# Optimization experiments

Hardware: AMD Instinct MI355X
Metric: run time of the kernel (lower is better)

## Reference

```python
import jax, jax.numpy as jnp
import numpy as np

V, D, N, M, H, W, K = 97, 512, 128, 64, 8, 8, 3
HALF = K // 2
DH = D // H
RPL = M + 3 + K   # key(M) + beta + gate + shift(K) + gamma = 70
WPL = RPL + 2 * M # + erase(M) + add(M) = 198
B, T = 32, 128


def _ln(x, g, b):
    mu = x.mean(-1, keepdims=True)
    var = ((x - mu) ** 2).mean(-1, keepdims=True)
    return (x - mu) / jnp.sqrt(var + 1e-5) * g + b


def _addressing(key, beta, gate, shift, gamma, prev_w, memory):
    # key [B,M], beta/gate/gamma [B,1], shift [B,K], prev_w [B,N], memory [B,N,M]
    eps = 1e-12
    kn = key / (jnp.linalg.norm(key, axis=-1, keepdims=True) + eps)
    mn = memory / (jnp.linalg.norm(memory, axis=-1, keepdims=True) + eps)
    cos = jnp.einsum('bnm,bm->bn', mn, kn)
    wc = jax.nn.softmax(jax.nn.softplus(beta) * cos, axis=-1)
    g = jax.nn.sigmoid(gate)
    wg = g * wc + (1.0 - g) * prev_w
    s = jax.nn.softmax(shift, axis=-1)
    shifted = sum(s[:, k:k + 1] * jnp.roll(wg, k - HALF, axis=-1) for k in range(K))
    gp = 1.0 + jax.nn.softplus(gamma)
    wt = (shifted + eps) ** gp
    return wt / (wt.sum(-1, keepdims=True) + eps)


def setup_inputs() -> dict:
    key = jax.random.key(0)
    ks = jax.random.split(key, 16)
    s = 0.05
    return {
        'x': jax.random.randint(ks[0], (B, T), 0, V),
        'emb': jax.random.normal(ks[1], (V, D)) * 0.02,
        'W_in': jax.random.normal(ks[2], (D, D + M)) * s,
        'b_in': jnp.zeros((D,)),
        'W_qkv': jax.random.normal(ks[3], (3 * D, D)) * s,
        'b_qkv': jnp.zeros((3 * D,)),
        'W_o': jax.random.normal(ks[4], (D, D)) * s,
        'b_o': jnp.zeros((D,)),
        'ln1_g': jnp.ones((D,)), 'ln1_b': jnp.zeros((D,)),
        'W_ff1': jax.random.normal(ks[5], (4 * D, D)) * s,
        'b_ff1': jnp.zeros((4 * D,)),
        'W_ff2': jax.random.normal(ks[6], (D, 4 * D)) * s,
        'b_ff2': jnp.zeros((D,)),
        'ln2_g': jnp.ones((D,)), 'ln2_b': jnp.zeros((D,)),
        'W_tok': jax.random.normal(ks[7], (V, D)) * s,
        'b_tok': jnp.zeros((V,)),
        'W_read': jax.random.normal(ks[8], (RPL, D)) * s,
        'b_read': jnp.zeros((RPL,)),
        'W_write': jax.random.normal(ks[9], (WPL, D)) * s,
        'b_write': jnp.zeros((WPL,)),
    }


def _forward(x, emb, W_in, b_in, W_qkv, b_qkv, W_o, b_o, ln1_g, ln1_b,
             W_ff1, b_ff1, W_ff2, b_ff2, ln2_g, ln2_b, W_tok, b_tok,
             W_read, b_read, W_write, b_write):
    Wq, Wk, Wv = W_qkv[:D], W_qkv[D:2 * D], W_qkv[2 * D:]
    bq, bk, bv = b_qkv[:D], b_qkv[D:2 * D], b_qkv[2 * D:]
    scale = 1.0 / np.sqrt(DH)

    def step(carry, x_t):
        memory, rw, ww, cache, t = carry
        tok = emb[x_t]                                   # [B,D]
        r = jnp.einsum('bn,bnm->bm', rw, memory)         # read vector [B,M]
        wide = jnp.concatenate([tok, r], -1)             # [B,D+M]
        xp = wide @ W_in.T + b_in                        # [B,D]
        q = xp[None]                                     # [1,B,D]
        # kv buffer: cache (detached) + current q, truncated to last W
        kbuf = jnp.concatenate([cache, q], 0)[-W:]       # [W,B,D]
        valid = jnp.arange(W) >= W - jnp.minimum(t + 1, W)
        qh = (xp @ Wq.T + bq).reshape(-1, H, DH)         # [B,H,DH]
        kh = (kbuf @ Wk.T + bk).reshape(W, -1, H, DH)    # [W,B,H,DH]
        vh = (kbuf @ Wv.T + bv).reshape(W, -1, H, DH)
        scores = jnp.einsum('bhe,wbhe->bhw', qh, kh) * scale
        scores = jnp.where(valid[None, None, :], scores, -jnp.inf)
        attn = jax.nn.softmax(scores, axis=-1)
        ctx = jnp.einsum('bhw,wbhe->bhe', attn, vh).reshape(-1, D)
        attn_out = ctx @ W_o.T + b_o
        x2 = _ln(xp + attn_out, ln1_g, ln1_b)
        ff = jax.nn.gelu(x2 @ W_ff1.T + b_ff1, approximate=False) @ W_ff2.T + b_ff2
        out = _ln(x2 + ff, ln2_g, ln2_b)
        logits = out @ W_tok.T + b_tok
        # read head addressing (RH=1)
        rp = out @ W_read.T + b_read
        new_rw = _addressing(rp[:, :M], rp[:, M:M + 1], rp[:, M + 1:M + 2],
                             rp[:, M + 2:M + 2 + K], rp[:, M + 2 + K:M + 3 + K],
                             rw, memory)
        # write head addressing + erase/add (WH=1)
        wp = out @ W_write.T + b_write
        new_ww = _addressing(wp[:, :M], wp[:, M:M + 1], wp[:, M + 1:M + 2],
                             wp[:, M + 2:M + 2 + K], wp[:, M + 2 + K:M + 3 + K],
                             ww, memory)
        erase = jax.nn.sigmoid(wp[:, RPL:RPL + M])       # [B,M]
        add = jnp.tanh(wp[:, RPL + M:])                  # [B,M]
        new_mem = memory * (1.0 - new_ww[:, :, None] * erase[:, None, :]) \
                  + new_ww[:, :, None] * add[:, None, :]
        new_cache = jax.lax.stop_gradient(jnp.concatenate([cache, q], 0)[-W:])
        return (new_mem, new_rw, new_ww, new_cache, t + 1), logits

    Bv = x.shape[0]
    mem0 = jnp.zeros((Bv, N, M), jnp.float32)
    w0 = jnp.zeros((Bv, N), jnp.float32).at[:, 0].set(1.0)
    cache0 = jnp.zeros((W, Bv, D), jnp.float32)
    carry0 = (mem0, w0, w0, cache0, jnp.int32(0))
    _, logits = jax.lax.scan(step, carry0, x.T)          # [T,B,V]
    return jnp.transpose(logits, (1, 0, 2))              # [B,T,V]


def reference(x, emb, W_in, b_in, W_qkv, b_qkv, W_o, b_o, ln1_g, ln1_b,
              W_ff1, b_ff1, W_ff2, b_ff2, ln2_g, ln2_b, W_tok, b_tok,
              W_read, b_read, W_write, b_write):
    return _forward(x, emb, W_in, b_in, W_qkv, b_qkv, W_o, b_o, ln1_g, ln1_b,
                    W_ff1, b_ff1, W_ff2, b_ff2, ln2_g, ln2_b, W_tok, b_tok,
                    W_read, b_read, W_write, b_write)
```

## Files before the change

### kernel.cpp

```cpp
#include <hip/hip_runtime.h>
#include <math.h>

static constexpr int Tc = 128, Vc = 97;

static constexpr size_t T_FQ  = 0;
static constexpr size_t BF    = T_FQ + (size_t)576*1536;
static constexpr size_t T_IN  = BF + 1536;
static constexpr size_t T_O   = T_IN + (size_t)576*512;
static constexpr size_t T_FF1 = T_O + (size_t)512*512;
static constexpr size_t T_FF2 = T_FF1 + (size_t)512*2048;
static constexpr size_t T_TOK = T_FF2 + (size_t)2048*512;
static constexpr size_t T_RW  = T_TOK + (size_t)512*128;
static constexpr size_t ARENA = T_RW + (size_t)512*288;
static constexpr size_t TEAM_STRIDE = 8704;
static constexpr size_t A_YP = 0;
static constexpr size_t A_OP = 4096;
static constexpr size_t A_RWP = 8192;
static constexpr size_t FLG = ARENA + (size_t)32*TEAM_STRIDE;

__device__ __forceinline__ float softplusf_(float x) { return x > 20.f ? x : log1pf(expf(x)); }
__device__ __forceinline__ float sigmoidf_(float x) { return 1.f / (1.f + expf(-x)); }

__device__ __forceinline__ float wsum(float v) {
#pragma unroll
  for (int o = 1; o < 64; o <<= 1) v += __shfl_xor(v, o);
  return v;
}
__device__ __forceinline__ float wmax(float v) {
#pragma unroll
  for (int o = 1; o < 64; o <<= 1) v = fmaxf(v, __shfl_xor(v, o));
  return v;
}

__device__ __forceinline__ void st_llc(float* p, float v) {
  __hip_atomic_store(p, v, __ATOMIC_RELAXED, __HIP_MEMORY_SCOPE_SYSTEM);
}
__device__ __forceinline__ float ld_llc(const float* p) {
  return __hip_atomic_load(p, __ATOMIC_RELAXED, __HIP_MEMORY_SCOPE_SYSTEM);
}
__device__ __forceinline__ void st_flag(int* p, int v) {
  __hip_atomic_store(p, v, __ATOMIC_RELAXED, __HIP_MEMORY_SCOPE_SYSTEM);
}
__device__ __forceinline__ int ld_flag(const int* p) {
  return __hip_atomic_load(p, __ATOMIC_RELAXED, __HIP_MEMORY_SCOPE_SYSTEM);
}

#define PUBF(stage)                                                      \
  do {                                                                   \
    asm volatile("s_waitcnt vmcnt(0)" ::: "memory");                     \
    __syncthreads();                                                     \
    if (tid == 0) st_flag(flg + (stage)*128 + sq*16, t + 1);             \
  } while (0)

#define WAITF(stage, need)                                               \
  do {                                                                   \
    if (tid < 8) {                                                       \
      while (ld_flag(flg + (stage)*128 + tid*16) < (need))               \
        __builtin_amdgcn_s_sleep(1);                                     \
    }                                                                    \
    __syncthreads();                                                     \
    asm volatile("" ::: "memory");                                       \
  } while (0)

template <int NCH, int CH, int NG, int SF4>
__device__ __forceinline__ void mvp(const float* __restrict__ wbase,
                                    const float* __restrict__ src,
                                    float* part, int tid) {
  const int cs = tid / NG, g = tid % NG;
  const float4* __restrict__ w4 =
      reinterpret_cast<const float4*>(wbase + (size_t)cs * CH * (SF4 * 4)) + g;
  const float* __restrict__ v = src + cs * CH;
  float a0 = 0.f, a1 = 0.f, a2 = 0.f, a3 = 0.f;
#pragma unroll 8
  for (int c = 0; c < CH; ++c) {
    float4 w = w4[(size_t)c * SF4];
    float vv = v[c];
    a0 += vv * w.x; a1 += vv * w.y; a2 += vv * w.z; a3 += vv * w.w;
  }
  *reinterpret_cast<float4*>(part + tid * 4) = make_float4(a0, a1, a2, a3);
}

__global__ __launch_bounds__(256) void k_init(const float* __restrict__ W_in,
                                              const float* __restrict__ W_qkv,
                                              const float* __restrict__ W_o,
                                              const float* __restrict__ W_ff1,
                                              const float* __restrict__ W_ff2,
                                              const float* __restrict__ W_tok,
                                              const float* __restrict__ W_read,
                                              const float* __restrict__ W_write,
                                              const float* __restrict__ b_qkv,
                                              const float* __restrict__ b_in,
                                              float* __restrict__ ws) {
  const size_t tid = (size_t)blockIdx.x * 256 + threadIdx.x;
  const size_t nth = (size_t)gridDim.x * 256;
  for (size_t i = tid; i < (size_t)576*512; i += nth) {
    size_t c = i >> 9, j = i & 511;
    ws[T_IN + i] = W_in[j * 576 + c];
  }
  for (size_t i = tid; i < (size_t)512*512; i += nth) {
    size_t e = i >> 9, j = i & 511;
    ws[T_O + i] = W_o[j * 512 + e];
  }
  for (size_t i = tid; i < (size_t)512*2048; i += nth) {
    size_t d = i >> 11, f = i & 2047;
    ws[T_FF1 + i] = W_ff1[f * 512 + d];
  }
  for (size_t i = tid; i < (size_t)2048*512; i += nth) {
    size_t k = i >> 9, j = i & 511;
    ws[T_FF2 + i] = W_ff2[j * 2048 + k];
  }
  for (size_t i = tid; i < (size_t)512*128; i += nth) {
    size_t d = i >> 7, j = i & 127;
    int qq = (int)(j >> 4), i2 = (int)(j & 15);
    int v = qq * 13 + i2;
    ws[T_TOK + i] = (i2 < 13 && v < 97) ? W_tok[(size_t)v * 512 + d] : 0.f;
  }
  for (size_t i = tid; i < (size_t)512*288; i += nth) {
    size_t d = i / 288, j = i % 288;
    int qq = (int)(j / 36), i2 = (int)(j % 36);
    int idx = qq * 34 + i2;
    float val = 0.f;
    if (i2 < 34 && idx < 268)
      val = (idx < 70) ? W_read[(size_t)idx * 512 + d] : W_write[(size_t)(idx - 70) * 512 + d];
    ws[T_RW + i] = val;
  }
  for (size_t j = tid; j < 1536; j += nth) {
    float a = b_qkv[j];
    const float* r = W_qkv + j * 512;
    for (int d = 0; d < 512; ++d) a += r[d] * b_in[d];
    ws[BF + j] = a;
  }
  for (size_t i = tid; i < (size_t)32 * TEAM_STRIDE; i += nth) ws[ARENA + i] = 0.f;
  for (size_t i = tid; i < 32768; i += nth) ((int*)(ws + FLG))[i] = 0;
}

__global__ __launch_bounds__(256) void k_fuse(const float* __restrict__ W_qkv,
                                              const float* __restrict__ W_in,
                                              float* __restrict__ ws) {
  __shared__ float As[32][64];
  __shared__ float Bs[32][96];
  const int cb = blockIdx.x % 9, jb = blockIdx.x / 9;
  const int c0 = cb * 64, j0 = jb * 96;
  const int tid = threadIdx.x;
  float acc[24];
#pragma unroll
  for (int u = 0; u < 24; ++u) acc[u] = 0.f;
  for (int d0 = 0; d0 < 512; d0 += 32) {
    __syncthreads();
    for (int i = tid; i < 32 * 64; i += 256) { int dd = i >> 6, cc = i & 63; As[dd][cc] = W_in[(size_t)(d0 + dd) * 576 + c0 + cc]; }
    for (int i = tid; i < 32 * 96; i += 256) { int jj = i >> 5, dd = i & 31; Bs[dd][jj] = W_qkv[(size_t)(j0 + jj) * 512 + d0 + dd]; }
    __syncthreads();
    const int tc = tid & 63, jbase = (tid >> 6) * 24;
    for (int dd = 0; dd < 32; ++dd) {
      float a = As[dd][tc];
#pragma unroll
      for (int u = 0; u < 24; ++u) acc[u] += a * Bs[dd][jbase + u];
    }
  }
  const int tc = tid & 63, jbase = (tid >> 6) * 24;
#pragma unroll
  for (int u = 0; u < 24; ++u)
    ws[T_FQ + (size_t)(c0 + tc) * 1536 + j0 + jbase + u] = acc[u];
}

__global__ __launch_bounds__(512) void k_main(
    const int* __restrict__ x, const float* __restrict__ emb,
    const float* __restrict__ b_in, const float* __restrict__ b_o,
    const float* __restrict__ ln1g, const float* __restrict__ ln1b,
    const float* __restrict__ b_ff1, const float* __restrict__ b_ff2,
    const float* __restrict__ ln2g, const float* __restrict__ ln2b,
    const float* __restrict__ b_tok,
    const float* __restrict__ b_read, const float* __restrict__ b_write,
    float* __restrict__ ws, float* __restrict__ dout) {
  const float* __restrict__ wt = ws;
  const int wg = blockIdx.x, tid = threadIdx.x;
  const int sq = wg & 7, b = wg >> 3;
  const int wv = tid >> 6, ln = tid & 63;
  float* ar = ws + ARENA + (size_t)b * TEAM_STRIDE;
  int* flg = (int*)(ws + FLG) + b * 1024;

  __shared__ float memS[128 * 64];
  __shared__ float kcS[8 * 64], vcS[8 * 64];
  __shared__ float rwvS[128], wwvS[128], wwnS[128];
  __shared__ float rvec[64];
  __shared__ float wideS[576];
  __shared__ float xpSl[64];
  __shared__ float qhS[64];
  __shared__ float scoresS[8], awS[8];
  __shared__ float ctxH[64];
  __shared__ float yS[512], x2S[512], oS[512], onS[512];
  __shared__ float hSl[256];
  __shared__ __align__(16) float part[2048];
  __shared__ float rwpS[272];
  __shared__ float cosS[256];
  __shared__ float redA[8], redB[8];
  __shared__ float eS[64], aS[64];

  for (int i = tid; i < 8192; i += 512) memS[i] = 0.f;
  if (tid < 128) { float v0 = (tid == 0) ? 1.f : 0.f; rwvS[tid] = v0; wwvS[tid] = v0; }
  __syncthreads();

  for (int t = 0; t < Tc; ++t) {
    {
      float a = 0.f;
#pragma unroll
      for (int k2 = 0; k2 < 16; ++k2) { int n = wv * 16 + k2; a += rwvS[n] * memS[n * 64 + ln]; }
      part[wv * 64 + ln] = a;
    }
    __syncthreads();
    if (tid < 64) {
      float s = 0.f;
#pragma unroll
      for (int p = 0; p < 8; ++p) s += part[p * 64 + tid];
      rvec[tid] = s;
    }
    __syncthreads();
    const int tok = x[b * Tc + t];
    for (int i = tid; i < 576; i += 512)
      wideS[i] = (i < 512) ? emb[(size_t)tok * 512 + i] : rvec[i - 512];
    __syncthreads();

    const int slot = t & 7;
    for (int p3 = 0; p3 < 3; ++p3) {
      mvp<32, 18, 16, 384>(wt + T_FQ + p3 * 512 + 64 * sq, wideS, part, tid);
      __syncthreads();
      if (tid < 64) {
        float s = wt[BF + p3 * 512 + 64 * sq + tid];
#pragma unroll
        for (int cs = 0; cs < 32; ++cs) s += part[cs * 64 + tid];
        if (p3 == 0) qhS[tid] = s;
        else if (p3 == 1) kcS[slot * 64 + tid] = s;
        else vcS[slot * 64 + tid] = s;
      }
      __syncthreads();
    }
    mvp<32, 18, 16, 128>(wt + T_IN + 64 * sq, wideS, part, tid);
    __syncthreads();
    if (tid < 64) {
      float s = b_in[64 * sq + tid];
#pragma unroll
      for (int cs = 0; cs < 32; ++cs) s += part[cs * 64 + tid];
      xpSl[tid] = s;
    }
    __syncthreads();

    {
      int st = t - 7 + wv;
      float c = 0.f;
      if (st >= 0) c = qhS[ln] * kcS[(st & 7) * 64 + ln];
      c = wsum(c);
      if (ln == 0) scoresS[wv] = (st >= 0) ? c * 0.125f : -INFINITY;
    }
    __syncthreads();
    if (tid == 0) {
      float mx = -INFINITY;
      for (int j = 0; j < 8; ++j) mx = fmaxf(mx, scoresS[j]);
      float e[8], ssum = 0.f;
      for (int j = 0; j < 8; ++j) { e[j] = expf(scoresS[j] - mx); ssum += e[j]; }
      float inv = 1.f / ssum;
      for (int j = 0; j < 8; ++j) awS[j] = e[j] * inv;
    }
    __syncthreads();
    if (tid < 64) {
      float a = 0.f;
#pragma unroll
      for (int j = 0; j < 8; ++j) {
        int st = t - 7 + j;
        if (st >= 0) a += awS[j] * vcS[(st & 7) * 64 + tid];
      }
      ctxH[tid] = a;
    }
    __syncthreads();

    mvp<4, 16, 128, 128>(wt + T_O + (size_t)64 * sq * 512, ctxH, part, tid);
    __syncthreads();
    {
      float s = 0.f;
#pragma unroll
      for (int cs = 0; cs < 4; ++cs) s += part[cs * 512 + tid];
      if ((tid >> 6) == sq) s += xpSl[tid & 63];
      st_llc(ar + A_YP + sq * 512 + tid, s);
    }
    PUBF(0);
    WAITF(0, t + 1);
    {
      float s = b_o[tid];
#pragma unroll
      for (int q2 = 0; q2 < 8; ++q2) s += ld_llc(ar + A_YP + q2 * 512 + tid);
      yS[tid] = s;
    }
    __syncthreads();
    {
      float v = yS[tid];
      float a = wsum(v), b2 = wsum(v * v);
      if (ln == 0) { redA[wv] = a; redB[wv] = b2; }
      __syncthreads();
      float sa = 0.f, sb = 0.f;
#pragma unroll
      for (int i2 = 0; i2 < 8; ++i2) { sa += redA[i2]; sb += redB[i2]; }
      float mu = sa * (1.f / 512.f);
      float var = sb * (1.f / 512.f) - mu * mu;
      float rstd = rsqrtf(var + 1e-5f);
      x2S[tid] = (yS[tid] - mu) * rstd * ln1g[tid] + ln1b[tid];
    }
    __syncthreads();

    mvp<8, 64, 64, 512>(wt + T_FF1 + 256 * sq, x2S, part, tid);
    __syncthreads();
    if (tid < 256) {
      float s = b_ff1[256 * sq + tid];
#pragma unroll
      for (int cs = 0; cs < 8; ++cs) s += part[cs * 256 + tid];
      hSl[tid] = 0.5f * s * (1.f + erff(s * 0.70710678118654752f));
    }
    __syncthreads();

    mvp<4, 64, 128, 128>(wt + T_FF2 + (size_t)256 * sq * 512, hSl, part, tid);
    __syncthreads();
    {
      float s = 0.f;
#pragma unroll
      for (int cs = 0; cs < 4; ++cs) s += part[cs * 512 + tid];
      st_llc(ar + A_OP + sq * 512 + tid, s);
    }
    PUBF(1);
    WAITF(1, t + 1);
    {
      float s = b_ff2[tid] + x2S[tid];
#pragma unroll
      for (int q2 = 0; q2 < 8; ++q2) s += ld_llc(ar + A_OP + q2 * 512 + tid);
      oS[tid] = s;
    }
    __syncthreads();
    {
      float v = oS[tid];
      float a = wsum(v), b2 = wsum(v * v);
      if (ln == 0) { redA[wv] = a; redB[wv] = b2; }
      __syncthreads();
      float sa = 0.f, sb = 0.f;
#pragma unroll
      for (int i2 = 0; i2 < 8; ++i2) { sa += redA[i2]; sb += redB[i2]; }
      float mu = sa * (1.f / 512.f);
      float var = sb * (1.f / 512.f) - mu * mu;
      float rstd = rsqrtf(var + 1e-5f);
      onS[tid] = (oS[tid] - mu) * rstd * ln2g[tid] + ln2b[tid];
    }
    __syncthreads();

    if (tid < 288) {
      const int cs = tid / 9, g = tid % 9;
      const float4* __restrict__ w4 =
          reinterpret_cast<const float4*>(wt + T_RW + (size_t)(cs * 16) * 288 + 36 * sq) + g;
      const float* __restrict__ v = onS + cs * 16;
      float a0 = 0.f, a1 = 0.f, a2 = 0.f, a3 = 0.f;
#pragma unroll
      for (int c = 0; c < 16; ++c) {
        float4 w = w4[(size_t)c * 72];
        float vv = v[c];
        a0 += vv * w.x; a1 += vv * w.y; a2 += vv * w.z; a3 += vv * w.w;
      }
      *reinterpret_cast<float4*>(part + cs * 36 + g * 4) = make_float4(a0, a1, a2, a3);
    }
    __syncthreads();
    if (tid < 34) {
      int idx = 34 * sq + tid;
      if (idx < 268) {
        float s = (idx < 70) ? b_read[idx] : b_write[idx - 70];
#pragma unroll
        for (int cs = 0; cs < 32; ++cs) s += part[cs * 36 + tid];
        st_llc(ar + A_RWP + idx, s);
      }
    }
    PUBF(2);
    if (tid < 128) {
      const int cs = tid >> 2, g = tid & 3;
      const float4* __restrict__ w4 =
          reinterpret_cast<const float4*>(wt + T_TOK + (size_t)(cs * 16) * 128 + 16 * sq) + g;
      const float* __restrict__ v = onS + cs * 16;
      float a0 = 0.f, a1 = 0.f, a2 = 0.f, a3 = 0.f;
#pragma unroll
      for (int c = 0; c < 16; ++c) {
        float4 w = w4[(size_t)c * 32];
        float vv = v[c];
        a0 += vv * w.x; a1 += vv * w.y; a2 += vv * w.z; a3 += vv * w.w;
      }
      *reinterpret_cast<float4*>(part + tid * 4) = make_float4(a0, a1, a2, a3);
    }
    __syncthreads();
    if (tid < 13) {
      int v = 13 * sq + tid;
      if (v < Vc) {
        float s = b_tok[v];
#pragma unroll
        for (int cs = 0; cs < 32; ++cs) s += part[cs * 16 + tid];
        dout[((size_t)b * Tc + t) * Vc + v] = s;
      }
    }
    WAITF(2, t + 1);
    if (tid < 268) rwpS[tid] = ld_llc(ar + A_RWP + tid);
    __syncthreads();

    for (int p = 0; p < 32; ++p) {
      int idx = wv * 32 + p;
      int ksel = idx >> 7, row = idx & 127;
      const float* key = ksel ? (rwpS + 70) : rwpS;
      float m = memS[row * 64 + ln];
      float pp = m * key[ln], qq = m * m;
#pragma unroll
      for (int o = 1; o < 64; o <<= 1) { pp += __shfl_xor(pp, o); qq += __shfl_xor(qq, o); }
      if (ln == 0) cosS[idx] = pp / (sqrtf(qq) + 1e-12f);
    }
    __syncthreads();
    if (wv < 2) {
      const float* P = wv ? (rwpS + 70) : rwpS;
      const float* cosb = cosS + wv * 128;
      float* prevw = wv ? wwvS : rwvS;
      float kk = P[ln];
      float kn2 = wsum(kk * kk);
      float kinv = 1.f / (sqrtf(kn2) + 1e-12f);
      float beta = softplusf_(P[64]);
      float g = sigmoidf_(P[65]);
      float sh0 = P[66], sh1 = P[67], sh2 = P[68];
      float m3 = fmaxf(sh0, fmaxf(sh1, sh2));
      float es0 = expf(sh0 - m3), es1 = expf(sh1 - m3), es2 = expf(sh2 - m3);
      float i3 = 1.f / (es0 + es1 + es2);
      es0 *= i3; es1 *= i3; es2 *= i3;
      float gp = 1.f + softplusf_(P[69]);
      float v0 = beta * cosb[ln] * kinv, v1 = beta * cosb[64 + ln] * kinv;
      float mx = wmax(fmaxf(v0, v1));
      float e0 = expf(v0 - mx), e1 = expf(v1 - mx);
      float einv = 1.f / wsum(e0 + e1);
      float w0 = g * e0 * einv + (1.f - g) * prevw[ln];
      float w1 = g * e1 * einv + (1.f - g) * prevw[64 + ln];
      float w0m = __shfl(w0, (ln + 63) & 63), w1m = __shfl(w1, (ln + 63) & 63);
      float w0p = __shfl(w0, (ln + 1) & 63),  w1p = __shfl(w1, (ln + 1) & 63);
      float prev0 = (ln == 0)  ? w1m : w0m;
      float next0 = (ln == 63) ? w1p : w0p;
      float prev1 = (ln == 0)  ? w0m : w1m;
      float next1 = (ln == 63) ? w0p : w1p;
      float t0 = es0 * next0 + es1 * w0 + es2 * prev0;
      float t1 = es0 * next1 + es1 * w1 + es2 * prev1;
      float wt0 = powf(t0 + 1e-12f, gp), wt1 = powf(t1 + 1e-12f, gp);
      float winv = 1.f / (wsum(wt0 + wt1) + 1e-12f);
      w0 = wt0 * winv; w1 = wt1 * winv;
      prevw[ln] = w0; prevw[64 + ln] = w1;
      if (wv) { wwnS[ln] = w0; wwnS[64 + ln] = w1; }
    } else if (wv == 2) {
      eS[ln] = sigmoidf_(rwpS[140 + ln]);
      aS[ln] = tanhf(rwpS[204 + ln]);
    }
    __syncthreads();
    for (int i = tid; i < 8192; i += 512) {
      int n = i >> 6, m = i & 63;
      float wn = wwnS[n];
      memS[i] = memS[i] * (1.f - wn * eS[m]) + wn * aS[m];
    }
    __syncthreads();
  }
}

extern "C" void kernel_launch(void* const* d_in, const int* in_sizes, int n_in,
                              void* d_out, int out_size, void* d_ws, size_t ws_size,
                              hipStream_t stream) {
  (void)in_sizes; (void)n_in; (void)out_size; (void)ws_size;
  const int* x = (const int*)d_in[0];
  const float* emb = (const float*)d_in[1];
  const float* W_in = (const float*)d_in[2];
  const float* b_in = (const float*)d_in[3];
  const float* W_qkv = (const float*)d_in[4];
  const float* b_qkv = (const float*)d_in[5];
  const float* W_o = (const float*)d_in[6];
  const float* b_o = (const float*)d_in[7];
  const float* ln1g = (const float*)d_in[8];
  const float* ln1b = (const float*)d_in[9];
  const float* W_ff1 = (const float*)d_in[10];
  const float* b_ff1 = (const float*)d_in[11];
  const float* W_ff2 = (const float*)d_in[12];
  const float* b_ff2 = (const float*)d_in[13];
  const float* ln2g = (const float*)d_in[14];
  const float* ln2b = (const float*)d_in[15];
  const float* W_tok = (const float*)d_in[16];
  const float* b_tok = (const float*)d_in[17];
  const float* W_read = (const float*)d_in[18];
  const float* b_read = (const float*)d_in[19];
  const float* W_write = (const float*)d_in[20];
  const float* b_write = (const float*)d_in[21];
  float* ws = (float*)d_ws;
  float* out = (float*)d_out;

  hipLaunchKernelGGL(k_init, dim3(512), dim3(256), 0, stream,
                     W_in, W_qkv, W_o, W_ff1, W_ff2, W_tok, W_read, W_write,
                     b_qkv, b_in, ws);
  hipLaunchKernelGGL(k_fuse, dim3(144), dim3(256), 0, stream, W_qkv, W_in, ws);
  hipLaunchKernelGGL(k_main, dim3(256), dim3(512), 0, stream,
                     x, emb, b_in, b_o, ln1g, ln1b, b_ff1, b_ff2,
                     ln2g, ln2b, b_tok, b_read, b_write, ws, out);
}
```

Baseline: 6.163 ms.

## Fuse QKV and input projections into one pass and batch weight loads

Merges the three Q/K/V matrix-vector passes and the W_in projection into a single loop, so each thread reads all four weight streams against the same input element. This cuts four rounds of sync-and-reduce down to one, and the partial-sum buffer grows to hold four outputs. The other matvecs now use a helper that issues eight float4 loads before doing the FMAs, which gives more memory-level parallelism. The launch bounds also ask for two blocks per CU, which can constrain registers and add spills. The larger shared-memory buffer may limit occupancy.

```diff
diff --git a/kernel.cpp b/kernel.cpp
--- a/kernel.cpp
+++ b/kernel.cpp
@@ -62,22 +62,28 @@
     asm volatile("" ::: "memory");                                       \
   } while (0)
 
-template <int NCH, int CH, int NG, int SF4>
-__device__ __forceinline__ void mvp(const float* __restrict__ wbase,
-                                    const float* __restrict__ src,
-                                    float* part, int tid) {
-  const int cs = tid / NG, g = tid % NG;
-  const float4* __restrict__ w4 =
-      reinterpret_cast<const float4*>(wbase + (size_t)cs * CH * (SF4 * 4)) + g;
-  const float* __restrict__ v = src + cs * CH;
+template <int CH, int SF4>
+__device__ __forceinline__ float4 dotw4(const float4* __restrict__ w4,
+                                        const float* __restrict__ v) {
   float a0 = 0.f, a1 = 0.f, a2 = 0.f, a3 = 0.f;
-#pragma unroll 8
-  for (int c = 0; c < CH; ++c) {
-    float4 w = w4[(size_t)c * SF4];
-    float vv = v[c];
+#pragma unroll
+  for (int c0 = 0; c0 + 8 <= CH; c0 += 8) {
+    float4 w[8];
+#pragma unroll
+    for (int j = 0; j < 8; ++j) w[j] = w4[(size_t)(c0 + j) * SF4];
+#pragma unroll
+    for (int j = 0; j < 8; ++j) {
+      float vv = v[c0 + j];
+      a0 += vv * w[j].x; a1 += vv * w[j].y; a2 += vv * w[j].z; a3 += vv * w[j].w;
+    }
+  }
+#pragma unroll
+  for (int cr = CH & ~7; cr < CH; ++cr) {
+    float4 w = w4[(size_t)cr * SF4];
+    float vv = v[cr];
     a0 += vv * w.x; a1 += vv * w.y; a2 += vv * w.z; a3 += vv * w.w;
   }
-  *reinterpret_cast<float4*>(part + tid * 4) = make_float4(a0, a1, a2, a3);
+  return make_float4(a0, a1, a2, a3);
 }
 
 __global__ __launch_bounds__(256) void k_init(const float* __restrict__ W_in,
@@ -163,7 +169,7 @@
     ws[T_FQ + (size_t)(c0 + tc) * 1536 + j0 + jbase + u] = acc[u];
 }
 
-__global__ __launch_bounds__(512) void k_main(
+__global__ __launch_bounds__(512, 2) void k_main(
     const int* __restrict__ x, const float* __restrict__ emb,
     const float* __restrict__ b_in, const float* __restrict__ b_o,
     const float* __restrict__ ln1g, const float* __restrict__ ln1b,
@@ -190,7 +196,7 @@
   __shared__ float ctxH[64];
   __shared__ float yS[512], x2S[512], oS[512], onS[512];
   __shared__ float hSl[256];
-  __shared__ __align__(16) float part[2048];
+  __shared__ __align__(16) float part[8192];
   __shared__ float rwpS[272];
   __shared__ float cosS[256];
   __shared__ float redA[8], redB[8];
@@ -221,33 +227,47 @@
     __syncthreads();
 
     const int slot = t & 7;
-    for (int p3 = 0; p3 < 3; ++p3) {
-      mvp<32, 18, 16, 384>(wt + T_FQ + p3 * 512 + 64 * sq, wideS, part, tid);
-      __syncthreads();
-      if (tid < 64) {
-        float s = wt[BF + p3 * 512 + 64 * sq + tid];
-#pragma unroll
-        for (int cs = 0; cs < 32; ++cs) s += part[cs * 64 + tid];
-        if (p3 == 0) qhS[tid] = s;
-        else if (p3 == 1) kcS[slot * 64 + tid] = s;
-        else vcS[slot * 64 + tid] = s;
+    {
+      const int cs = tid >> 4, g = tid & 15;
+      const float4* __restrict__ fq4 = reinterpret_cast<const float4*>(wt + T_FQ + 64 * sq);
+      const float4* __restrict__ in4 = reinterpret_cast<const float4*>(wt + T_IN + 64 * sq);
+      float4 aq = make_float4(0.f, 0.f, 0.f, 0.f);
+      float4 ak = aq, av = aq, ax = aq;
+      const int c0 = cs * 18;
+#pragma unroll 6
+      for (int c = 0; c < 18; ++c) {
+        const size_t ro = (size_t)(c0 + c);
+        float4 wq = fq4[ro * 384 + g];
+        float4 wk = fq4[ro * 384 + 128 + g];
+        float4 wv2 = fq4[ro * 384 + 256 + g];
+        float4 wx = in4[ro * 128 + g];
+        float vv = wideS[c0 + c];
+        aq.x += vv * wq.x;  aq.y += vv * wq.y;  aq.z += vv * wq.z;  aq.w += vv * wq.w;
+        ak.x += vv * wk.x;  ak.y += vv * wk.y;  ak.z += vv * wk.z;  ak.w += vv * wk.w;
+        av.x += vv * wv2.x; av.y += vv * wv2.y; av.z += vv * wv2.z; av.w += vv * wv2.w;
+        ax.x += vv * wx.x;  ax.y += vv * wx.y;  ax.z += vv * wx.z;  ax.w += vv * wx.w;
       }
-      __syncthreads();
-    }
-    mvp<32, 18, 16, 128>(wt + T_IN + 64 * sq, wideS, part, tid);
-    __syncthreads();
-    if (tid < 64) {
-      float s = b_in[64 * sq + tid];
-#pragma unroll
-      for (int cs = 0; cs < 32; ++cs) s += part[cs * 64 + tid];
-      xpSl[tid] = s;
+      *reinterpret_cast<float4*>(part + 0 * 2048 + tid * 4) = aq;
+      *reinterpret_cast<float4*>(part + 1 * 2048 + tid * 4) = ak;
+      *reinterpret_cast<float4*>(part + 2 * 2048 + tid * 4) = av;
+      *reinterpret_cast<float4*>(part + 3 * 2048 + tid * 4) = ax;
+    }
+    __syncthreads();
+    if (tid < 256) {
+      const int ph = tid >> 6, j = tid & 63;
+      float s = 0.f;
+#pragma unroll
+      for (int cs2 = 0; cs2 < 32; ++cs2) s += part[ph * 2048 + cs2 * 64 + j];
+      if (ph == 0) qhS[j] = s + wt[BF + 64 * sq + j];
+      else if (ph == 1) kcS[slot * 64 + j] = s + wt[BF + 512 + 64 * sq + j];
+      else if (ph == 2) vcS[slot * 64 + j] = s + wt[BF + 1024 + 64 * sq + j];
+      else xpSl[j] = s + b_in[64 * sq + j];
     }
     __syncthreads();
 
     {
       int st = t - 7 + wv;
-      float c = 0.f;
-      if (st >= 0) c = qhS[ln] * kcS[(st & 7) * 64 + ln];
+      float c = (st >= 0) ? qhS[ln] * kcS[(st & 7) * 64 + ln] : 0.f;
       c = wsum(c);
       if (ln == 0) scoresS[wv] = (st >= 0) ? c * 0.125f : -INFINITY;
     }
@@ -272,7 +292,13 @@
     }
     __syncthreads();
 
-    mvp<4, 16, 128, 128>(wt + T_O + (size_t)64 * sq * 512, ctxH, part, tid);
+    {
+      const int cs = tid >> 7, g = tid & 127;
+      const float4* __restrict__ w4 =
+          reinterpret_cast<const float4*>(wt + T_O + ((size_t)64 * sq + cs * 16) * 512) + g;
+      float4 a4 = dotw4<16, 128>(w4, ctxH + cs * 16);
+      *reinterpret_cast<float4*>(part + tid * 4) = a4;
+    }
     __syncthreads();
     {
       float s = 0.f;
@@ -305,7 +331,13 @@
     }
     __syncthreads();
 
-    mvp<8, 64, 64, 512>(wt + T_FF1 + 256 * sq, x2S, part, tid);
+    {
+      const int cs = tid >> 6, g = tid & 63;
+      const float4* __restrict__ w4 =
+          reinterpret_cast<const float4*>(wt + T_FF1 + (size_t)(cs * 64) * 2048 + 256 * sq) + g;
+      float4 a4 = dotw4<64, 512>(w4, x2S + cs * 64);
+      *reinterpret_cast<float4*>(part + tid * 4) = a4;
+    }
     __syncthreads();
     if (tid < 256) {
       float s = b_ff1[256 * sq + tid];
@@ -315,7 +347,13 @@
     }
     __syncthreads();
 
-    mvp<4, 64, 128, 128>(wt + T_FF2 + (size_t)256 * sq * 512, hSl, part, tid);
+    {
+      const int cs = tid >> 7, g = tid & 127;
+      const float4* __restrict__ w4 =
+          reinterpret_cast<const float4*>(wt + T_FF2 + ((size_t)256 * sq + cs * 64) * 512) + g;
+      float4 a4 = dotw4<64, 128>(w4, hSl + cs * 64);
+      *reinterpret_cast<float4*>(part + tid * 4) = a4;
+    }
     __syncthreads();
     {
       float s = 0.f;
@@ -351,15 +389,8 @@
       const int cs = tid / 9, g = tid % 9;
       const float4* __restrict__ w4 =
           reinterpret_cast<const float4*>(wt + T_RW + (size_t)(cs * 16) * 288 + 36 * sq) + g;
-      const float* __restrict__ v = onS + cs * 16;
-      float a0 = 0.f, a1 = 0.f, a2 = 0.f, a3 = 0.f;
-#pragma unroll
-      for (int c = 0; c < 16; ++c) {
-        float4 w = w4[(size_t)c * 72];
-        float vv = v[c];
-        a0 += vv * w.x; a1 += vv * w.y; a2 += vv * w.z; a3 += vv * w.w;
-      }
-      *reinterpret_cast<float4*>(part + cs * 36 + g * 4) = make_float4(a0, a1, a2, a3);
+      float4 a4 = dotw4<16, 72>(w4, onS + cs * 16);
+      *reinterpret_cast<float4*>(part + cs * 36 + g * 4) = a4;
     }
     __syncthreads();
     if (tid < 34) {
@@ -376,15 +407,8 @@
       const int cs = tid >> 2, g = tid & 3;
       const float4* __restrict__ w4 =
           reinterpret_cast<const float4*>(wt + T_TOK + (size_t)(cs * 16) * 128 + 16 * sq) + g;
-      const float* __restrict__ v = onS + cs * 16;
-      float a0 = 0.f, a1 = 0.f, a2 = 0.f, a3 = 0.f;
-#pragma unroll
-      for (int c = 0; c < 16; ++c) {
-        float4 w = w4[(size_t)c * 32];
-        float vv = v[c];
-        a0 += vv * w.x; a1 += vv * w.y; a2 += vv * w.z; a3 += vv * w.w;
-      }
-      *reinterpret_cast<float4*>(part + tid * 4) = make_float4(a0, a1, a2, a3);
+      float4 a4 = dotw4<16, 32>(w4, onS + cs * 16);
+      *reinterpret_cast<float4*>(part + tid * 4) = a4;
     }
     __syncthreads();
     if (tid < 13) {
```

New measurement: 13.18 ms. 114% more time.
